# Performance work log

Measured on AMD Instinct MI355X. Metric: run time of the kernel, lower is better.

## Reference

```python
import jax, jax.numpy as jnp
import numpy as np

EPS = 1e-5  # F.instance_norm default eps


def _patch_attn(x, s):
    """Per-(b,c) instance norm over non-overlapping s x s patches, then sigmoid."""
    b, c, h, w = x.shape
    xr = x.reshape(b, c, h // s, s, w // s, s)
    m = jnp.mean(xr, axis=(3, 5), keepdims=True)
    v = jnp.mean((xr - m) ** 2, axis=(3, 5), keepdims=True)  # biased var, as in training-mode instance_norm
    a = jax.nn.sigmoid((xr - m) * jax.lax.rsqrt(v + EPS))
    return a.reshape(b, c, h, w)


def setup_inputs() -> dict:
    key = jax.random.key(0)
    x = jax.random.normal(key, (16, 64, 256, 256), dtype=jnp.float32)
    return {"x": x}


def reference(x):
    p = (2, 1, 0)
    b, c, h, w = x.shape
    out = x
    for pi in p:  # fixed 3 scales (structural loop, not data loop)
        s = h // (2 ** pi)
        attn = _patch_attn(out, s)
        out = 0.5 * out + 0.5 * (attn * out)
    return out
```

## Files before the change

kernel.cpp:

```cpp
#include <hip/hip_runtime.h>

#define PEPS 1e-5f

__device__ __forceinline__ float fast_rcp(float x) { return __builtin_amdgcn_rcpf(x); }

__device__ __forceinline__ float patch_one(float x, float m, float rs) {
    const float e = __expf((m - x) * rs);
    return x * fmaf(0.5f, fast_rcp(1.0f + e), 0.5f);
}

__device__ __forceinline__ void wave_reduce2(float& a, float& b) {
#pragma unroll
    for (int off = 32; off; off >>= 1) {
        a += __shfl_xor(a, off);
        b += __shfl_xor(b, off);
    }
}

__global__ __launch_bounds__(1024) void fused_pyramid(const float* __restrict__ in,
                                                      float* __restrict__ out)
{
    constexpr int W = 256;
    const int tid  = threadIdx.x;
    const int wave = tid >> 6;
    const int lane = tid & 63;
    const int pr   = wave >> 2;
    const int pc   = wave & 3;
    const size_t base = (size_t)blockIdx.x * (W * W) + (size_t)(pr * 64) * W + pc * 64;

    __shared__ float redS[16], redQ[16];

    float4 v[16];
    float s = 0.f, q = 0.f;
#pragma unroll
    for (int u = 0; u < 16; ++u) {
        const int j  = u * 64 + lane;
        const int r  = j >> 4;
        const int c4 = j & 15;
        const float4 t = *reinterpret_cast<const float4*>(in + base + (size_t)r * W + c4 * 4);
        v[u] = t;
        s += (t.x + t.y) + (t.z + t.w);
        q = fmaf(t.x, t.x, fmaf(t.y, t.y, fmaf(t.z, t.z, fmaf(t.w, t.w, q))));
    }

    wave_reduce2(s, q);
    float m  = s * (1.0f / 4096.0f);
    float rs = rsqrtf(fmaf(-m, m, q * (1.0f / 4096.0f)) + PEPS);

    float s2 = 0.f, q2 = 0.f;
#pragma unroll
    for (int u = 0; u < 16; ++u) {
        float4 t = v[u];
        t.x = patch_one(t.x, m, rs);
        t.y = patch_one(t.y, m, rs);
        t.z = patch_one(t.z, m, rs);
        t.w = patch_one(t.w, m, rs);
        v[u] = t;
        s2 += (t.x + t.y) + (t.z + t.w);
        q2 = fmaf(t.x, t.x, fmaf(t.y, t.y, fmaf(t.z, t.z, fmaf(t.w, t.w, q2))));
    }

    wave_reduce2(s2, q2);
    if (lane == 0) { redS[wave] = s2; redQ[wave] = q2; }
    __syncthreads();
    const int w00 = wave & ~5;
    {
        const float S = (redS[w00] + redS[w00 + 1]) + (redS[w00 + 4] + redS[w00 + 5]);
        const float Q = (redQ[w00] + redQ[w00 + 1]) + (redQ[w00 + 4] + redQ[w00 + 5]);
        m  = S * (1.0f / 16384.0f);
        rs = rsqrtf(fmaf(-m, m, Q * (1.0f / 16384.0f)) + PEPS);
    }

    float s3 = 0.f, q3 = 0.f;
#pragma unroll
    for (int u = 0; u < 16; ++u) {
        float4 t = v[u];
        t.x = patch_one(t.x, m, rs);
        t.y = patch_one(t.y, m, rs);
        t.z = patch_one(t.z, m, rs);
        t.w = patch_one(t.w, m, rs);
        v[u] = t;
        s3 += (t.x + t.y) + (t.z + t.w);
        q3 = fmaf(t.x, t.x, fmaf(t.y, t.y, fmaf(t.z, t.z, fmaf(t.w, t.w, q3))));
    }

    wave_reduce2(s3, q3);
    __syncthreads();
    if (lane == 0) { redS[wave] = s3; redQ[wave] = q3; }
    __syncthreads();
    {
        float S = 0.f, Q = 0.f;
#pragma unroll
        for (int w = 0; w < 16; ++w) { S += redS[w]; Q += redQ[w]; }
        m  = S * (1.0f / 65536.0f);
        rs = rsqrtf(fmaf(-m, m, Q * (1.0f / 65536.0f)) + PEPS);
    }

#pragma unroll
    for (int u = 0; u < 16; ++u) {
        const int j  = u * 64 + lane;
        const int r  = j >> 4;
        const int c4 = j & 15;
        float4 t = v[u];
        t.x = patch_one(t.x, m, rs);
        t.y = patch_one(t.y, m, rs);
        t.z = patch_one(t.z, m, rs);
        t.w = patch_one(t.w, m, rs);
        *reinterpret_cast<float4*>(out + base + (size_t)r * W + c4 * 4) = t;
    }
}

extern "C" void kernel_launch(void* const* d_in, const int* in_sizes, int n_in,
                              void* d_out, int out_size, void* d_ws, size_t ws_size,
                              hipStream_t stream)
{
    const float* x = (const float*)d_in[0];
    float* out = (float*)d_out;
    constexpr int IMGS = 16 * 64;
    fused_pyramid<<<IMGS, 1024, 0, stream>>>(x, out);
}
```

Before: 127.0 us.

## Split each image across two blocks with global atomic handshake, fold sigmoid into exp2

Each 256x256 image is now handled by two 512-thread blocks, one per half, instead of one 1024-thread block. The final whole-image statistics are combined through atomics in workspace and a spin-wait flag. The sigmoid argument is also prefolded into a single fma followed by a native exp2. The split is meant to raise occupancy and scheduling flexibility, at the cost of an extra memset launch and a risk of spin-wait deadlock if the paired block is not co-resident.

Measured after the change: 215.5 us. 69.7% more time.

```diff
diff --git a/kernel.cpp b/kernel.cpp
--- a/kernel.cpp
+++ b/kernel.cpp
@@ -1,11 +1,12 @@
 #include <hip/hip_runtime.h>
 
-#define PEPS 1e-5f
+#define PEPS  1e-5f
+#define LOG2E 1.4426950408889634f
 
 __device__ __forceinline__ float fast_rcp(float x) { return __builtin_amdgcn_rcpf(x); }
 
-__device__ __forceinline__ float patch_one(float x, float m, float rs) {
-    const float e = __expf((m - x) * rs);
+__device__ __forceinline__ float patch_one(float x, float nrs2, float mrs) {
+    const float e = __builtin_amdgcn_exp2f(fmaf(x, nrs2, mrs));
     return x * fmaf(0.5f, fast_rcp(1.0f + e), 0.5f);
 }
 
@@ -17,18 +18,21 @@
     }
 }
 
-__global__ __launch_bounds__(1024) void fused_pyramid(const float* __restrict__ in,
-                                                      float* __restrict__ out)
+__global__ __launch_bounds__(512, 4) void fused_pyramid_half(
+    const float* __restrict__ in, float* __restrict__ out, float* __restrict__ ws)
 {
     constexpr int W = 256;
     const int tid  = threadIdx.x;
     const int wave = tid >> 6;
     const int lane = tid & 63;
+    const int img  = blockIdx.x >> 1;
+    const int half = blockIdx.x & 1;
     const int pr   = wave >> 2;
     const int pc   = wave & 3;
-    const size_t base = (size_t)blockIdx.x * (W * W) + (size_t)(pr * 64) * W + pc * 64;
+    const size_t base = (size_t)img * (W * W) + (size_t)half * (128 * W)
+                      + (size_t)(pr * 64) * W + pc * 64;
 
-    __shared__ float redS[16], redQ[16];
+    __shared__ float redS[8], redQ[8], stats[2];
 
     float4 v[16];
     float s = 0.f, q = 0.f;
@@ -46,15 +50,17 @@
     wave_reduce2(s, q);
     float m  = s * (1.0f / 4096.0f);
     float rs = rsqrtf(fmaf(-m, m, q * (1.0f / 4096.0f)) + PEPS);
+    float nrs2 = rs * -LOG2E;
+    float mrs  = m * rs * LOG2E;
 
     float s2 = 0.f, q2 = 0.f;
 #pragma unroll
     for (int u = 0; u < 16; ++u) {
         float4 t = v[u];
-        t.x = patch_one(t.x, m, rs);
-        t.y = patch_one(t.y, m, rs);
-        t.z = patch_one(t.z, m, rs);
-        t.w = patch_one(t.w, m, rs);
+        t.x = patch_one(t.x, nrs2, mrs);
+        t.y = patch_one(t.y, nrs2, mrs);
+        t.z = patch_one(t.z, nrs2, mrs);
+        t.w = patch_one(t.w, nrs2, mrs);
         v[u] = t;
         s2 += (t.x + t.y) + (t.z + t.w);
         q2 = fmaf(t.x, t.x, fmaf(t.y, t.y, fmaf(t.z, t.z, fmaf(t.w, t.w, q2))));
@@ -70,15 +76,17 @@
         m  = S * (1.0f / 16384.0f);
         rs = rsqrtf(fmaf(-m, m, Q * (1.0f / 16384.0f)) + PEPS);
     }
+    nrs2 = rs * -LOG2E;
+    mrs  = m * rs * LOG2E;
 
     float s3 = 0.f, q3 = 0.f;
 #pragma unroll
     for (int u = 0; u < 16; ++u) {
         float4 t = v[u];
-        t.x = patch_one(t.x, m, rs);
-        t.y = patch_one(t.y, m, rs);
-        t.z = patch_one(t.z, m, rs);
-        t.w = patch_one(t.w, m, rs);
+        t.x = patch_one(t.x, nrs2, mrs);
+        t.y = patch_one(t.y, nrs2, mrs);
+        t.z = patch_one(t.z, nrs2, mrs);
+        t.w = patch_one(t.w, nrs2, mrs);
         v[u] = t;
         s3 += (t.x + t.y) + (t.z + t.w);
         q3 = fmaf(t.x, t.x, fmaf(t.y, t.y, fmaf(t.z, t.z, fmaf(t.w, t.w, q3))));
@@ -88,13 +96,29 @@
     __syncthreads();
     if (lane == 0) { redS[wave] = s3; redQ[wave] = q3; }
     __syncthreads();
-    {
+    if (tid == 0) {
         float S = 0.f, Q = 0.f;
 #pragma unroll
-        for (int w = 0; w < 16; ++w) { S += redS[w]; Q += redQ[w]; }
-        m  = S * (1.0f / 65536.0f);
-        rs = rsqrtf(fmaf(-m, m, Q * (1.0f / 65536.0f)) + PEPS);
+        for (int w = 0; w < 8; ++w) { S += redS[w]; Q += redQ[w]; }
+        float* slot = ws + (size_t)img * 4;
+        atomicAdd(slot + 0, S);
+        atomicAdd(slot + 1, Q);
+        __threadfence();
+        unsigned* flag = reinterpret_cast<unsigned*>(slot + 2);
+        atomicAdd(flag, 1u);
+        while (__hip_atomic_load(flag, __ATOMIC_ACQUIRE, __HIP_MEMORY_SCOPE_AGENT) < 2u)
+            __builtin_amdgcn_s_sleep(1);
+        const float St = __hip_atomic_load(slot + 0, __ATOMIC_RELAXED, __HIP_MEMORY_SCOPE_AGENT);
+        const float Qt = __hip_atomic_load(slot + 1, __ATOMIC_RELAXED, __HIP_MEMORY_SCOPE_AGENT);
+        const float mm = St * (1.0f / 65536.0f);
+        stats[0] = mm;
+        stats[1] = rsqrtf(fmaf(-mm, mm, Qt * (1.0f / 65536.0f)) + PEPS);
     }
+    __syncthreads();
+    m  = stats[0];
+    rs = stats[1];
+    nrs2 = rs * -LOG2E;
+    mrs  = m * rs * LOG2E;
 
 #pragma unroll
     for (int u = 0; u < 16; ++u) {
@@ -102,10 +126,10 @@
         const int r  = j >> 4;
         const int c4 = j & 15;
         float4 t = v[u];
-        t.x = patch_one(t.x, m, rs);
-        t.y = patch_one(t.y, m, rs);
-        t.z = patch_one(t.z, m, rs);
-        t.w = patch_one(t.w, m, rs);
+        t.x = patch_one(t.x, nrs2, mrs);
+        t.y = patch_one(t.y, nrs2, mrs);
+        t.z = patch_one(t.z, nrs2, mrs);
+        t.w = patch_one(t.w, nrs2, mrs);
         *reinterpret_cast<float4*>(out + base + (size_t)r * W + c4 * 4) = t;
     }
 }
@@ -117,5 +141,8 @@
     const float* x = (const float*)d_in[0];
     float* out = (float*)d_out;
     constexpr int IMGS = 16 * 64;
-    fused_pyramid<<<IMGS, 1024, 0, stream>>>(x, out);
+
+    hipMemsetAsync(d_ws, 0, (size_t)IMGS * 4 * sizeof(float), stream);
+
+    fused_pyramid_half<<<IMGS * 2, 512, 0, stream>>>(x, out, (float*)d_ws);
 }
```
